# Kernel optimization log

Measured on AMD Instinct MI355X. Metric: run time of the kernel, lower is better.

## Reference

```python
import jax, jax.numpy as jnp
import numpy as np

N_NODES = 100000
N_EDGES = 3200000


def _gcn_norm(row, col, n):
    # GCNConv default: add self loops, sym norm D^-1/2 (A+I) D^-1/2
    loop = jnp.arange(n, dtype=row.dtype)
    r = jnp.concatenate([row, loop])
    c = jnp.concatenate([col, loop])
    deg = jax.ops.segment_sum(jnp.ones_like(r, dtype=jnp.float32), r, num_segments=n)
    dinv = jnp.where(deg > 0, jax.lax.rsqrt(deg), 0.0)
    norm = dinv[r] * dinv[c]  # [E+N]
    return r, c, norm


def _gcn_conv(x, W, b, r, c, norm, n):
    h = x @ W  # dense transform first (in > out)
    msg = h[c] * norm[:, None]  # gather sources, scale
    out = jax.ops.segment_sum(msg, r, num_segments=n)  # scatter to destinations
    return out + b


def setup_inputs() -> dict:
    key = jax.random.key(0)
    ks = jax.random.split(key, 5)
    x = jax.random.normal(ks[0], (N_NODES, 1433), dtype=jnp.float32)
    row = jax.random.randint(ks[1], (N_EDGES,), 0, N_NODES, dtype=jnp.int32)
    col = jax.random.randint(ks[2], (N_EDGES,), 0, N_NODES, dtype=jnp.int32)
    W1 = jax.random.normal(ks[3], (1433, 16), dtype=jnp.float32) * (1.0 / np.sqrt(1433))
    b1 = jnp.zeros((16,), dtype=jnp.float32)
    W2 = jax.random.normal(ks[4], (16, 7), dtype=jnp.float32) * (1.0 / np.sqrt(16))
    b2 = jnp.zeros((7,), dtype=jnp.float32)
    return {"x": x, "row": row, "col": col, "W1": W1, "b1": b1, "W2": W2, "b2": b2}


def reference(x, row, col, W1, b1, W2, b2):
    n = x.shape[0]
    r, c, norm = _gcn_norm(row, col, n)
    h = _gcn_conv(x, W1, b1, r, c, norm, n)
    h = jax.nn.relu(h)
    # dropout is identity in eval mode (reference is deterministic)
    h = _gcn_conv(h, W2, b2, r, c, norm, n)
    return jax.nn.log_softmax(h, axis=1)
```

## Files before the change

### kernel.cpp

```cpp
#include <hip/hip_runtime.h>
#include <math.h>

#define N_NODES 100000
#define N_EDGES 3200000
#define FIN     1433

__global__ void k_zero(int* __restrict__ p, int n) {
  int i = blockIdx.x * blockDim.x + threadIdx.x;
  if (i < n) p[i] = 0;
}

__global__ void k_hist(const int* __restrict__ row, int* __restrict__ cnt) {
  int e = blockIdx.x * blockDim.x + threadIdx.x;
  if (e < N_EDGES) atomicAdd(&cnt[row[e]], 1);
}

__global__ void k_dinv(const int* __restrict__ cnt, float* __restrict__ dinv) {
  int i = blockIdx.x * blockDim.x + threadIdx.x;
  if (i < N_NODES) dinv[i] = 1.0f / sqrtf((float)(cnt[i] + 1));
}

__global__ void k_scanA(const int* __restrict__ cnt, int* __restrict__ bsum) {
  __shared__ int sd[256];
  int t = threadIdx.x, b = blockIdx.x;
  int base = b * 1024 + t * 4;
  int s = 0;
#pragma unroll
  for (int m = 0; m < 4; m++) {
    int i = base + m;
    if (i < N_NODES) s += cnt[i];
  }
  sd[t] = s; __syncthreads();
  for (int off = 128; off > 0; off >>= 1) {
    if (t < off) sd[t] += sd[t + off];
    __syncthreads();
  }
  if (t == 0) bsum[b] = sd[0];
}

__global__ void k_scanB(int* __restrict__ bsum, int* __restrict__ rowStart, int nb) {
  __shared__ int sd[128];
  int t = threadIdx.x;
  int v = (t < nb) ? bsum[t] : 0;
  sd[t] = v;
  __syncthreads();
  for (int off = 1; off < 128; off <<= 1) {
    int add = (t >= off) ? sd[t - off] : 0;
    __syncthreads();
    sd[t] += add;
    __syncthreads();
  }
  if (t < nb) bsum[t] = (t == 0) ? 0 : sd[t - 1];
  if (t == 0) rowStart[N_NODES] = sd[nb - 1];
}

__global__ void k_scanC(const int* __restrict__ cnt, const int* __restrict__ bsum,
                        int* __restrict__ rowStart) {
  __shared__ int sd[256];
  int t = threadIdx.x, b = blockIdx.x;
  int base = b * 1024 + t * 4;
  int v[4], pre[4], s = 0;
#pragma unroll
  for (int m = 0; m < 4; m++) {
    int i = base + m;
    v[m] = (i < N_NODES) ? cnt[i] : 0;
    pre[m] = s; s += v[m];
  }
  sd[t] = s; __syncthreads();
  for (int off = 1; off < 256; off <<= 1) {
    int add = (t >= off) ? sd[t - off] : 0;
    __syncthreads();
    sd[t] += add;
    __syncthreads();
  }
  int ex = (t == 0) ? 0 : sd[t - 1];
  int base0 = bsum[b] + ex;
#pragma unroll
  for (int m = 0; m < 4; m++) {
    int i = base + m;
    if (i < N_NODES) rowStart[i] = base0 + pre[m];
  }
}

__global__ void k_scatter(const int* __restrict__ row, const int* __restrict__ col,
                          const int* __restrict__ rowStart, int* __restrict__ fill,
                          int* __restrict__ colc) {
  int e = blockIdx.x * blockDim.x + threadIdx.x;
  if (e < N_EDGES) {
    int r = row[e];
    int pos = rowStart[r] + atomicAdd(&fill[r], 1);
    colc[pos] = col[e];
  }
}

__global__ __launch_bounds__(64) void k_gemm1(const float* __restrict__ x,
                                              const float* __restrict__ W1,
                                              float* __restrict__ t1) {
  int rowi = blockIdx.x * 64 + threadIdx.x;
  if (rowi >= N_NODES) return;
  const float* __restrict__ xr = x + (size_t)rowi * FIN;

  float acc[16];
#pragma unroll
  for (int j = 0; j < 16; j++) acc[j] = 0.0f;

  float4 buf[8], nbuf[8];
#pragma unroll
  for (int m = 0; m < 8; m++) buf[m] = *(const float4*)(xr + m * 4);

  const int NCH = 44;
  for (int ch = 0; ch < NCH; ch++) {
    int kc = ch * 32;
    if (ch + 1 < NCH) {
#pragma unroll
      for (int m = 0; m < 8; m++) nbuf[m] = *(const float4*)(xr + kc + 32 + m * 4);
    }
#pragma unroll
    for (int m = 0; m < 8; m++) {
      float xv0 = buf[m].x, xv1 = buf[m].y, xv2 = buf[m].z, xv3 = buf[m].w;
      const float* w0 = &W1[(size_t)(kc + m * 4 + 0) * 16];
      const float* w1 = &W1[(size_t)(kc + m * 4 + 1) * 16];
      const float* w2 = &W1[(size_t)(kc + m * 4 + 2) * 16];
      const float* w3 = &W1[(size_t)(kc + m * 4 + 3) * 16];
#pragma unroll
      for (int j = 0; j < 16; j++) {
        acc[j] = fmaf(xv0, w0[j], acc[j]);
        acc[j] = fmaf(xv1, w1[j], acc[j]);
        acc[j] = fmaf(xv2, w2[j], acc[j]);
        acc[j] = fmaf(xv3, w3[j], acc[j]);
      }
    }
#pragma unroll
    for (int m = 0; m < 8; m++) buf[m] = nbuf[m];
  }
  for (int k = 1408; k < FIN; k++) {
    float xv = xr[k];
    const float* w = &W1[(size_t)k * 16];
#pragma unroll
    for (int j = 0; j < 16; j++) acc[j] = fmaf(xv, w[j], acc[j]);
  }

  float* o = t1 + (size_t)rowi * 16;
#pragma unroll
  for (int j = 0; j < 16; j += 4)
    *(float4*)(o + j) = make_float4(acc[j], acc[j + 1], acc[j + 2], acc[j + 3]);
}

__global__ __launch_bounds__(256) void k_agg1(const float* __restrict__ t1,
                                              const int* __restrict__ rowStart,
                                              const int* __restrict__ colc,
                                              const float* __restrict__ dinv,
                                              const float* __restrict__ b1,
                                              float* __restrict__ h1r) {
  int lane = threadIdx.x & 63;
  int wid  = threadIdx.x >> 6;
  int node = blockIdx.x * 4 + wid;
  if (node >= N_NODES) return;
  int q = lane & 3, slot = lane >> 2;
  int s0 = rowStart[node], s1 = rowStart[node + 1];
  float ax = 0.f, ay = 0.f, az = 0.f, aw = 0.f;
  for (int e = s0 + slot; e < s1; e += 16) {
    int c = colc[e];
    float w = dinv[c];
    float4 v = *(const float4*)(t1 + (size_t)c * 16 + q * 4);
    ax = fmaf(v.x, w, ax); ay = fmaf(v.y, w, ay);
    az = fmaf(v.z, w, az); aw = fmaf(v.w, w, aw);
  }
#pragma unroll
  for (int off = 4; off < 64; off <<= 1) {
    ax += __shfl_xor(ax, off, 64);
    ay += __shfl_xor(ay, off, 64);
    az += __shfl_xor(az, off, 64);
    aw += __shfl_xor(aw, off, 64);
  }
  float di = dinv[node];
  if (slot == 0) {
    float4 sv = *(const float4*)(t1 + (size_t)node * 16 + q * 4);
    float4 bb = *(const float4*)(b1 + q * 4);
    float4 o;
    o.x = fmaxf(0.f, di * (ax + di * sv.x) + bb.x);
    o.y = fmaxf(0.f, di * (ay + di * sv.y) + bb.y);
    o.z = fmaxf(0.f, di * (az + di * sv.z) + bb.z);
    o.w = fmaxf(0.f, di * (aw + di * sv.w) + bb.w);
    *(float4*)(h1r + (size_t)node * 16 + q * 4) = o;
  }
}

__global__ void k_gemm2(const float* __restrict__ h1r, const float* __restrict__ W2,
                        float* __restrict__ t2) {
  int i = blockIdx.x * blockDim.x + threadIdx.x;
  if (i >= N_NODES) return;
  float h[16];
#pragma unroll
  for (int k = 0; k < 16; k++) h[k] = h1r[(size_t)i * 16 + k];
  float a[7] = {0, 0, 0, 0, 0, 0, 0};
#pragma unroll
  for (int k = 0; k < 16; k++)
#pragma unroll
    for (int j = 0; j < 7; j++) a[j] = fmaf(h[k], W2[k * 7 + j], a[j]);
  float* o = t2 + (size_t)i * 8;
#pragma unroll
  for (int j = 0; j < 7; j++) o[j] = a[j];
  o[7] = 0.0f;
}

__global__ __launch_bounds__(256) void k_agg2(const float* __restrict__ t2,
                                              const int* __restrict__ rowStart,
                                              const int* __restrict__ colc,
                                              const float* __restrict__ dinv,
                                              const float* __restrict__ b2,
                                              float* __restrict__ out) {
  int lane = threadIdx.x & 63;
  int wid  = threadIdx.x >> 6;
  int node = blockIdx.x * 4 + wid;
  if (node >= N_NODES) return;
  int q = lane & 1, slot = lane >> 1;
  int s0 = rowStart[node], s1 = rowStart[node + 1];
  float ax = 0.f, ay = 0.f, az = 0.f, aw = 0.f;
  for (int e = s0 + slot; e < s1; e += 32) {
    int c = colc[e];
    float w = dinv[c];
    float4 v = *(const float4*)(t2 + (size_t)c * 8 + q * 4);
    ax = fmaf(v.x, w, ax); ay = fmaf(v.y, w, ay);
    az = fmaf(v.z, w, az); aw = fmaf(v.w, w, aw);
  }
#pragma unroll
  for (int off = 2; off < 64; off <<= 1) {
    ax += __shfl_xor(ax, off, 64);
    ay += __shfl_xor(ay, off, 64);
    az += __shfl_xor(az, off, 64);
    aw += __shfl_xor(aw, off, 64);
  }
  float di = dinv[node];
  float4 sv = *(const float4*)(t2 + (size_t)node * 8 + q * 4);
  float lg[4];
  float am[4] = {ax, ay, az, aw};
  float sm[4] = {sv.x, sv.y, sv.z, sv.w};
#pragma unroll
  for (int m = 0; m < 4; m++) {
    int j = 4 * q + m;
    float bb = (j < 7) ? b2[j] : 0.0f;
    lg[m] = di * (am[m] + di * sm[m]) + bb;
    if (j == 7) lg[m] = -1e30f;
  }
  float o4 = __shfl_xor(lg[0], 1, 64);
  float o5 = __shfl_xor(lg[1], 1, 64);
  float o6 = __shfl_xor(lg[2], 1, 64);
  if (lane == 0) {
    float a[7] = {lg[0], lg[1], lg[2], lg[3], o4, o5, o6};
    float mx = a[0];
#pragma unroll
    for (int j = 1; j < 7; j++) mx = fmaxf(mx, a[j]);
    float s = 0.f;
#pragma unroll
    for (int j = 0; j < 7; j++) s += expf(a[j] - mx);
    float lse = mx + logf(s);
    float* o = out + (size_t)node * 7;
#pragma unroll
    for (int j = 0; j < 7; j++) o[j] = a[j] - lse;
  }
}

extern "C" void kernel_launch(void* const* d_in, const int* in_sizes, int n_in,
                              void* d_out, int out_size, void* d_ws, size_t ws_size,
                              hipStream_t stream) {
  const float* x   = (const float*)d_in[0];
  const int*   row = (const int*)d_in[1];
  const int*   col = (const int*)d_in[2];
  const float* W1  = (const float*)d_in[3];
  const float* b1  = (const float*)d_in[4];
  const float* W2  = (const float*)d_in[5];
  const float* b2  = (const float*)d_in[6];
  float* out = (float*)d_out;

  char* w = (char*)d_ws;
  auto alloc = [&](size_t bytes) {
    char* p = w;
    w += (bytes + 255) & ~(size_t)255;
    return p;
  };
  int*   cnt      = (int*)alloc((size_t)N_NODES * 4);
  int*   fill     = (int*)alloc((size_t)N_NODES * 4);
  int*   rowStart = (int*)alloc((size_t)(N_NODES + 1) * 4);
  int*   bsum     = (int*)alloc(128 * 4);
  float* dinv     = (float*)alloc((size_t)N_NODES * 4);
  int*   colc     = (int*)alloc((size_t)N_EDGES * 4);
  float* t1       = (float*)alloc((size_t)N_NODES * 16 * 4);
  float* h1r      = (float*)alloc((size_t)N_NODES * 16 * 4);
  float* t2       = (float*)alloc((size_t)N_NODES * 8 * 4);

  const int NB = (N_NODES + 1023) / 1024;

  k_zero<<<(N_NODES + 255) / 256, 256, 0, stream>>>(cnt, N_NODES);
  k_zero<<<(N_NODES + 255) / 256, 256, 0, stream>>>(fill, N_NODES);
  k_hist<<<(N_EDGES + 255) / 256, 256, 0, stream>>>(row, cnt);
  k_dinv<<<(N_NODES + 255) / 256, 256, 0, stream>>>(cnt, dinv);
  k_scanA<<<NB, 256, 0, stream>>>(cnt, bsum);
  k_scanB<<<1, 128, 0, stream>>>(bsum, rowStart, NB);
  k_scanC<<<NB, 256, 0, stream>>>(cnt, bsum, rowStart);
  k_scatter<<<(N_EDGES + 255) / 256, 256, 0, stream>>>(row, col, rowStart, fill, colc);
  k_gemm1<<<(N_NODES + 63) / 64, 64, 0, stream>>>(x, W1, t1);
  k_agg1<<<(N_NODES + 3) / 4, 256, 0, stream>>>(t1, rowStart, colc, dinv, b1, h1r);
  k_gemm2<<<(N_NODES + 255) / 256, 256, 0, stream>>>(h1r, W2, t2);
  k_agg2<<<(N_NODES + 3) / 4, 256, 0, stream>>>(t2, rowStart, colc, dinv, b2, out);
}
```

Before: 1.214 ms.

## Fold source-degree scaling into transforms, fuse gemm2 into agg1, vectorize CSR build

Pre-scales each node's transformed features by its own dinv in gemm1 and in agg1's output, so the aggregation loops drop the per-edge dinv gather and do plain sums. The second dense transform (16x7) is fused into the epilogue of agg1 with a shuffle reduction across the four feature quads, which removes the k_gemm2 kernel and the h1r round trip. The CSR build folds dinv computation and fill-pointer initialisation into scanC, which drops two launches, and reads row/col as int4 in hist and scatter. Summation order changes slightly, and the code assumes N_EDGES is divisible by 4 and that the input buffers are 16-byte aligned.

```diff
diff --git a/kernel.cpp b/kernel.cpp
--- a/kernel.cpp
+++ b/kernel.cpp
@@ -10,14 +10,15 @@
   if (i < n) p[i] = 0;
 }
 
-__global__ void k_hist(const int* __restrict__ row, int* __restrict__ cnt) {
-  int e = blockIdx.x * blockDim.x + threadIdx.x;
-  if (e < N_EDGES) atomicAdd(&cnt[row[e]], 1);
-}
-
-__global__ void k_dinv(const int* __restrict__ cnt, float* __restrict__ dinv) {
+__global__ void k_hist(const int4* __restrict__ row4, int* __restrict__ cnt) {
   int i = blockIdx.x * blockDim.x + threadIdx.x;
-  if (i < N_NODES) dinv[i] = 1.0f / sqrtf((float)(cnt[i] + 1));
+  if (i < N_EDGES / 4) {
+    int4 r = row4[i];
+    atomicAdd(&cnt[r.x], 1);
+    atomicAdd(&cnt[r.y], 1);
+    atomicAdd(&cnt[r.z], 1);
+    atomicAdd(&cnt[r.w], 1);
+  }
 }
 
 __global__ void k_scanA(const int* __restrict__ cnt, int* __restrict__ bsum) {
@@ -55,7 +56,8 @@
 }
 
 __global__ void k_scanC(const int* __restrict__ cnt, const int* __restrict__ bsum,
-                        int* __restrict__ rowStart) {
+                        int* __restrict__ rowStart, int* __restrict__ fillpos,
+                        float* __restrict__ dinv) {
   __shared__ int sd[256];
   int t = threadIdx.x, b = blockIdx.x;
   int base = b * 1024 + t * 4;
@@ -78,24 +80,32 @@
 #pragma unroll
   for (int m = 0; m < 4; m++) {
     int i = base + m;
-    if (i < N_NODES) rowStart[i] = base0 + pre[m];
-  }
-}
-
-__global__ void k_scatter(const int* __restrict__ row, const int* __restrict__ col,
-                          const int* __restrict__ rowStart, int* __restrict__ fill,
-                          int* __restrict__ colc) {
-  int e = blockIdx.x * blockDim.x + threadIdx.x;
-  if (e < N_EDGES) {
-    int r = row[e];
-    int pos = rowStart[r] + atomicAdd(&fill[r], 1);
-    colc[pos] = col[e];
+    if (i < N_NODES) {
+      int rs = base0 + pre[m];
+      rowStart[i] = rs;
+      fillpos[i]  = rs;
+      dinv[i] = 1.0f / sqrtf((float)(v[m] + 1));
+    }
+  }
+}
+
+__global__ void k_scatter(const int4* __restrict__ row4, const int4* __restrict__ col4,
+                          int* __restrict__ fillpos, int* __restrict__ colc) {
+  int i = blockIdx.x * blockDim.x + threadIdx.x;
+  if (i < N_EDGES / 4) {
+    int4 r = row4[i];
+    int4 c = col4[i];
+    int p0 = atomicAdd(&fillpos[r.x], 1); colc[p0] = c.x;
+    int p1 = atomicAdd(&fillpos[r.y], 1); colc[p1] = c.y;
+    int p2 = atomicAdd(&fillpos[r.z], 1); colc[p2] = c.z;
+    int p3 = atomicAdd(&fillpos[r.w], 1); colc[p3] = c.w;
   }
 }
 
 __global__ __launch_bounds__(64) void k_gemm1(const float* __restrict__ x,
                                               const float* __restrict__ W1,
-                                              float* __restrict__ t1) {
+                                              const float* __restrict__ dinv,
+                                              float* __restrict__ t1s) {
   int rowi = blockIdx.x * 64 + threadIdx.x;
   if (rowi >= N_NODES) return;
   const float* __restrict__ xr = x + (size_t)rowi * FIN;
@@ -140,18 +150,21 @@
     for (int j = 0; j < 16; j++) acc[j] = fmaf(xv, w[j], acc[j]);
   }
 
-  float* o = t1 + (size_t)rowi * 16;
+  float di = dinv[rowi];
+  float* o = t1s + (size_t)rowi * 16;
 #pragma unroll
   for (int j = 0; j < 16; j += 4)
-    *(float4*)(o + j) = make_float4(acc[j], acc[j + 1], acc[j + 2], acc[j + 3]);
-}
-
-__global__ __launch_bounds__(256) void k_agg1(const float* __restrict__ t1,
+    *(float4*)(o + j) = make_float4(di * acc[j], di * acc[j + 1],
+                                    di * acc[j + 2], di * acc[j + 3]);
+}
+
+__global__ __launch_bounds__(256) void k_agg1(const float* __restrict__ t1s,
                                               const int* __restrict__ rowStart,
                                               const int* __restrict__ colc,
                                               const float* __restrict__ dinv,
                                               const float* __restrict__ b1,
-                                              float* __restrict__ h1r) {
+                                              const float* __restrict__ W2,
+                                              float* __restrict__ t2s) {
   int lane = threadIdx.x & 63;
   int wid  = threadIdx.x >> 6;
   int node = blockIdx.x * 4 + wid;
@@ -161,10 +174,8 @@
   float ax = 0.f, ay = 0.f, az = 0.f, aw = 0.f;
   for (int e = s0 + slot; e < s1; e += 16) {
     int c = colc[e];
-    float w = dinv[c];
-    float4 v = *(const float4*)(t1 + (size_t)c * 16 + q * 4);
-    ax = fmaf(v.x, w, ax); ay = fmaf(v.y, w, ay);
-    az = fmaf(v.z, w, az); aw = fmaf(v.w, w, aw);
+    float4 v = *(const float4*)(t1s + (size_t)c * 16 + q * 4);
+    ax += v.x; ay += v.y; az += v.z; aw += v.w;
   }
 #pragma unroll
   for (int off = 4; off < 64; off <<= 1) {
@@ -175,36 +186,36 @@
   }
   float di = dinv[node];
   if (slot == 0) {
-    float4 sv = *(const float4*)(t1 + (size_t)node * 16 + q * 4);
+    float4 sv = *(const float4*)(t1s + (size_t)node * 16 + q * 4);
     float4 bb = *(const float4*)(b1 + q * 4);
-    float4 o;
-    o.x = fmaxf(0.f, di * (ax + di * sv.x) + bb.x);
-    o.y = fmaxf(0.f, di * (ay + di * sv.y) + bb.y);
-    o.z = fmaxf(0.f, di * (az + di * sv.z) + bb.z);
-    o.w = fmaxf(0.f, di * (aw + di * sv.w) + bb.w);
-    *(float4*)(h1r + (size_t)node * 16 + q * 4) = o;
-  }
-}
-
-__global__ void k_gemm2(const float* __restrict__ h1r, const float* __restrict__ W2,
-                        float* __restrict__ t2) {
-  int i = blockIdx.x * blockDim.x + threadIdx.x;
-  if (i >= N_NODES) return;
-  float h[16];
-#pragma unroll
-  for (int k = 0; k < 16; k++) h[k] = h1r[(size_t)i * 16 + k];
-  float a[7] = {0, 0, 0, 0, 0, 0, 0};
-#pragma unroll
-  for (int k = 0; k < 16; k++)
-#pragma unroll
-    for (int j = 0; j < 7; j++) a[j] = fmaf(h[k], W2[k * 7 + j], a[j]);
-  float* o = t2 + (size_t)i * 8;
-#pragma unroll
-  for (int j = 0; j < 7; j++) o[j] = a[j];
-  o[7] = 0.0f;
-}
-
-__global__ __launch_bounds__(256) void k_agg2(const float* __restrict__ t2,
+    float h0 = fmaxf(0.f, di * (ax + sv.x) + bb.x);
+    float h1 = fmaxf(0.f, di * (ay + sv.y) + bb.y);
+    float h2 = fmaxf(0.f, di * (az + sv.z) + bb.z);
+    float h3 = fmaxf(0.f, di * (aw + sv.w) + bb.w);
+    float p[8];
+#pragma unroll
+    for (int j = 0; j < 8; j++) p[j] = 0.f;
+    const float* w = W2 + q * 4 * 7;
+#pragma unroll
+    for (int j = 0; j < 7; j++)
+      p[j] = h0 * w[j] + h1 * w[7 + j] + h2 * w[14 + j] + h3 * w[21 + j];
+#pragma unroll
+    for (int off = 1; off < 4; off <<= 1) {
+#pragma unroll
+      for (int j = 0; j < 7; j++) p[j] += __shfl_xor(p[j], off, 64);
+    }
+    if (q < 2) {
+      float4 o;
+      o.x = di * p[q * 4 + 0];
+      o.y = di * p[q * 4 + 1];
+      o.z = di * p[q * 4 + 2];
+      o.w = di * p[q * 4 + 3];
+      *(float4*)(t2s + (size_t)node * 8 + q * 4) = o;
+    }
+  }
+}
+
+__global__ __launch_bounds__(256) void k_agg2(const float* __restrict__ t2s,
                                               const int* __restrict__ rowStart,
                                               const int* __restrict__ colc,
                                               const float* __restrict__ dinv,
@@ -219,10 +230,8 @@
   float ax = 0.f, ay = 0.f, az = 0.f, aw = 0.f;
   for (int e = s0 + slot; e < s1; e += 32) {
     int c = colc[e];
-    float w = dinv[c];
-    float4 v = *(const float4*)(t2 + (size_t)c * 8 + q * 4);
-    ax = fmaf(v.x, w, ax); ay = fmaf(v.y, w, ay);
-    az = fmaf(v.z, w, az); aw = fmaf(v.w, w, aw);
+    float4 v = *(const float4*)(t2s + (size_t)c * 8 + q * 4);
+    ax += v.x; ay += v.y; az += v.z; aw += v.w;
   }
 #pragma unroll
   for (int off = 2; off < 64; off <<= 1) {
@@ -232,7 +241,7 @@
     aw += __shfl_xor(aw, off, 64);
   }
   float di = dinv[node];
-  float4 sv = *(const float4*)(t2 + (size_t)node * 8 + q * 4);
+  float4 sv = *(const float4*)(t2s + (size_t)node * 8 + q * 4);
   float lg[4];
   float am[4] = {ax, ay, az, aw};
   float sm[4] = {sv.x, sv.y, sv.z, sv.w};
@@ -240,7 +249,7 @@
   for (int m = 0; m < 4; m++) {
     int j = 4 * q + m;
     float bb = (j < 7) ? b2[j] : 0.0f;
-    lg[m] = di * (am[m] + di * sm[m]) + bb;
+    lg[m] = di * (am[m] + sm[m]) + bb;
     if (j == 7) lg[m] = -1e30f;
   }
   float o4 = __shfl_xor(lg[0], 1, 64);
@@ -280,27 +289,25 @@
     return p;
   };
   int*   cnt      = (int*)alloc((size_t)N_NODES * 4);
-  int*   fill     = (int*)alloc((size_t)N_NODES * 4);
+  int*   fillpos  = (int*)alloc((size_t)N_NODES * 4);
   int*   rowStart = (int*)alloc((size_t)(N_NODES + 1) * 4);
   int*   bsum     = (int*)alloc(128 * 4);
   float* dinv     = (float*)alloc((size_t)N_NODES * 4);
   int*   colc     = (int*)alloc((size_t)N_EDGES * 4);
-  float* t1       = (float*)alloc((size_t)N_NODES * 16 * 4);
-  float* h1r      = (float*)alloc((size_t)N_NODES * 16 * 4);
-  float* t2       = (float*)alloc((size_t)N_NODES * 8 * 4);
+  float* t1s      = (float*)alloc((size_t)N_NODES * 16 * 4);
+  float* t2s      = (float*)alloc((size_t)N_NODES * 8 * 4);
 
   const int NB = (N_NODES + 1023) / 1024;
+  const int E4 = N_EDGES / 4;
 
   k_zero<<<(N_NODES + 255) / 256, 256, 0, stream>>>(cnt, N_NODES);
-  k_zero<<<(N_NODES + 255) / 256, 256, 0, stream>>>(fill, N_NODES);
-  k_hist<<<(N_EDGES + 255) / 256, 256, 0, stream>>>(row, cnt);
-  k_dinv<<<(N_NODES + 255) / 256, 256, 0, stream>>>(cnt, dinv);
+  k_hist<<<(E4 + 255) / 256, 256, 0, stream>>>((const int4*)row, cnt);
   k_scanA<<<NB, 256, 0, stream>>>(cnt, bsum);
   k_scanB<<<1, 128, 0, stream>>>(bsum, rowStart, NB);
-  k_scanC<<<NB, 256, 0, stream>>>(cnt, bsum, rowStart);
-  k_scatter<<<(N_EDGES + 255) / 256, 256, 0, stream>>>(row, col, rowStart, fill, colc);
-  k_gemm1<<<(N_NODES + 63) / 64, 64, 0, stream>>>(x, W1, t1);
-  k_agg1<<<(N_NODES + 3) / 4, 256, 0, stream>>>(t1, rowStart, colc, dinv, b1, h1r);
-  k_gemm2<<<(N_NODES + 255) / 256, 256, 0, stream>>>(h1r, W2, t2);
-  k_agg2<<<(N_NODES + 3) / 4, 256, 0, stream>>>(t2, rowStart, colc, dinv, b2, out);
-}
+  k_scanC<<<NB, 256, 0, stream>>>(cnt, bsum, rowStart, fillpos, dinv);
+  k_scatter<<<(E4 + 255) / 256, 256, 0, stream>>>((const int4*)row, (const int4*)col,
+                                                  fillpos, colc);
+  k_gemm1<<<(N_NODES + 63) / 64, 64, 0, stream>>>(x, W1, dinv, t1s);
+  k_agg1<<<(N_NODES + 3) / 4, 256, 0, stream>>>(t1s, rowStart, colc, dinv, b1, W2, t2s);
+  k_agg2<<<(N_NODES + 3) / 4, 256, 0, stream>>>(t2s, rowStart, colc, dinv, b2, out);
+}
```

Measured after the change: 1.319 ms. 8.7% more time.
